# Optimization experiments

Measured on AMD Instinct MI355X. Metric: run time of the kernel, lower is better.

Reference implementation:

```python
import jax, jax.numpy as jnp
import numpy as np

NF = 3
THRESH = 0.05
MODES1 = [0, 64, 32]
MODES2 = [0, 64, 32]
LEVEL = 3
WIDTHS = [32, 64, 64]


def _cgelu(z):
    # split-complex GELU: gelu on real and imag parts independently
    return jax.nn.gelu(z.real) + 1j * jax.nn.gelu(z.imag)


def _forward(x_real, x_imag, Re,
             p_w1_r, p_w1_i, p_b1_r, p_b1_i, p_w2_r, p_w2_i, p_b2_r, p_b2_i,
             w0_r, w0_i, wd1_r, wd1_i, wu1_r, wu1_i, wd2_r, wd2_i, wu2_r, wu2_i,
             S1, S2):
    c = lambda r, i: (r + 1j * i).astype(jnp.complex64)
    x = c(x_real, x_imag)                       # (B, C0, S1, M2) half-spectrum
    B = x.shape[0]
    M1, M2 = S1 // 2, S2 // 2 + 1
    m1_list = [M1, MODES1[1], MODES1[2]]
    m2_list = [M2, MODES2[1], MODES2[2]]

    # --- get_k: fractional powers of signed wavenumbers ---
    h1, h2 = S1 // 2, S2 // 2
    kx1 = jnp.concatenate([jnp.arange(0, S1 - h1), jnp.arange(-h1, 0)]).reshape(S1, 1)
    kx2 = jnp.concatenate([jnp.arange(0, S2 - h2), jnp.arange(-h2, 0)]).reshape(1, S2)
    k = jnp.stack([jnp.broadcast_to(kx1, (S1, S2)),
                   jnp.broadcast_to(kx2, (S1, S2))], 0)[..., :M2]   # (2, S1, M2)
    pw = (jnp.arange(1, NF + 1, dtype=jnp.float32) / NF).reshape(NF, 1, 1, 1)
    k_mat = jnp.power(k[None].astype(jnp.complex64), pw)            # (NF, 2, S1, M2)
    k_mat = jnp.broadcast_to(k_mat.reshape(1, 2 * NF, S1, M2), (B, 2 * NF, S1, M2))

    # --- embed_re: fractional powers of Reynolds number ---
    re_pw = (jnp.arange(1, NF + 1, dtype=jnp.float32) / NF).reshape(1, NF, 1, 1)
    re_mat = jnp.power(Re, re_pw).astype(jnp.complex64)             # (B, NF, 1, 1)
    re_mat = jnp.broadcast_to(re_mat, (B, NF, S1, M2))

    feat = jnp.concatenate([k_mat, re_mat], axis=1)                 # (B, 3*NF, S1, M2)

    # --- complex 1x1-conv MLP p ---
    h = jnp.einsum('bixy,oi->boxy', feat, c(p_w1_r, p_w1_i)) + c(p_b1_r, p_b1_i)[None, :, None, None]
    h = _cgelu(h)
    re_feature = jnp.einsum('bixy,oi->boxy', h, c(p_w2_r, p_w2_i)) + c(p_b2_r, p_b2_i)[None, :, None, None]

    x = x * re_feature
    x = jnp.where(jnp.abs(x) > THRESH, x, jnp.zeros((), x.dtype))   # sparsity mask

    # level 0 (skip_in is all-ones complex)
    x1 = x + 1.0
    x1 = _cgelu(jnp.einsum('bixy,io->boxy', x1, c(w0_r, w0_i)))

    Wd = [None, c(wd1_r, wd1_i), c(wd2_r, wd2_i)]
    Wu = [None, c(wu1_r, wu1_i), c(wu2_r, wu2_i)]

    xs = [x1]
    for i in range(1, LEVEL):  # down path: corner mode truncation + channel mix
        m1, m2 = m1_list[i], m2_list[i]
        x2 = jnp.concatenate([x1[:, :, :m1, :m2], x1[:, :, -m1:, :m2]], axis=2)
        x1 = _cgelu(jnp.einsum('bixy,io->boxy', x2, Wd[i])) + 1.0
        xs.append(x1)

    skip_out = list(xs)
    for i in range(LEVEL - 1, 0, -1):  # up path: channel mix + corner add
        u = _cgelu(jnp.einsum('bixy,io->boxy', xs[i], Wu[i]))
        m1, m2 = m1_list[i], m2_list[i]
        prev = xs[i - 1]
        prev = prev.at[:, :, :m1, :m2].add(u[:, :, :m1, :m2])
        prev = prev.at[:, :, -m1:, :m2].add(u[:, :, -m1:, :m2])
        xs[i - 1] = prev
        skip_out[i - 1] = prev  # torch mutates in place, so skip_out aliases

    return (xs[0], skip_out[0], skip_out[1], skip_out[2])


def setup_inputs() -> dict:
    key = jax.random.key(0)
    B, S1, S2 = 8, 256, 256
    M2 = S2 // 2 + 1
    ks = jax.random.split(key, 24)
    f = lambda k, s: jax.random.normal(k, s, jnp.float32)
    w = lambda k, s: 0.05 * jax.random.normal(k, s, jnp.float32)
    return {
        'x_real': f(ks[0], (B, 32, S1, M2)),
        'x_imag': f(ks[1], (B, 32, S1, M2)),
        'Re': jax.random.uniform(ks[2], (B, 1, 1, 1), jnp.float32, 0.5, 2.0),
        'p_w1_r': w(ks[3], (32, 9)), 'p_w1_i': w(ks[4], (32, 9)),
        'p_b1_r': w(ks[5], (32,)), 'p_b1_i': w(ks[6], (32,)),
        'p_w2_r': w(ks[7], (32, 32)), 'p_w2_i': w(ks[8], (32, 32)),
        'p_b2_r': w(ks[9], (32,)), 'p_b2_i': w(ks[10], (32,)),
        'w0_r': w(ks[11], (32, 32)), 'w0_i': w(ks[12], (32, 32)),
        'wd1_r': w(ks[13], (32, 64)), 'wd1_i': w(ks[14], (32, 64)),
        'wu1_r': w(ks[15], (64, 32)), 'wu1_i': w(ks[16], (64, 32)),
        'wd2_r': w(ks[17], (64, 64)), 'wd2_i': w(ks[18], (64, 64)),
        'wu2_r': w(ks[19], (64, 64)), 'wu2_i': w(ks[20], (64, 64)),
        'S1': S1, 'S2': S2,
    }


def reference(x_real, x_imag, Re,
              p_w1_r, p_w1_i, p_b1_r, p_b1_i, p_w2_r, p_w2_i, p_b2_r, p_b2_i,
              w0_r, w0_i, wd1_r, wd1_i, wu1_r, wu1_i, wd2_r, wd2_i, wu2_r, wu2_i,
              S1, S2):
    return _forward(x_real, x_imag, Re,
                    p_w1_r, p_w1_i, p_b1_r, p_b1_i, p_w2_r, p_w2_i, p_b2_r, p_b2_i,
                    w0_r, w0_i, wd1_r, wd1_i, wu1_r, wu1_i, wd2_r, wd2_i, wu2_r, wu2_i,
                    S1, S2)
```

## Files before the change

### kernel.cpp

```cpp
#include <hip/hip_runtime.h>

typedef long long i64;

#define BB   8
#define SS1  256
#define MM2  129
#define SP0  (SS1*MM2)

#define O0 0LL
#define O1 8454144LL
#define O2 16908288LL
#define O3 21102592LL

__device__ __forceinline__ float ldf(const float* p, i64 i, i64 cap) {
    return (i >= 0 && i < cap) ? p[i] : 0.0f;
}
__device__ __forceinline__ void stf(float* p, i64 i, i64 cap, float v) {
    if (i >= 0 && i < cap) p[i] = v;
}

__device__ __forceinline__ float tanh_fast(float x) {
    float a = fabsf(x);
    float t = __expf(-2.0f * a);
    float r = (1.0f - t) / (1.0f + t);
    return copysignf(r, x);
}
__device__ __forceinline__ float gelu_f(float x) {
    float inner = 0.7978845608028654f * (x + 0.044715f * x * x * x);
    return 0.5f * x * (1.0f + tanh_fast(inner));
}

__device__ __forceinline__ void compute_features(
    int b, int x, int y, const float* __restrict__ Re,
    float* fr, float* fi, float* rp)
{
    float kv0 = (x < 128) ? (float)x : (float)(x - 256);
    float kv1 = (y < 128) ? (float)y : -128.0f;
    const float P[3] = {1.0f/3.0f, 2.0f/3.0f, 1.0f};
    #pragma unroll
    for (int d = 0; d < 2; d++) {
        float k = d ? kv1 : kv0;
        float lg = __logf(fabsf(k));
        #pragma unroll
        for (int f = 0; f < 3; f++) {
            int c = f * 2 + d;
            float m = __expf(P[f] * lg);
            if (k == 0.0f)      { fr[c] = 0.0f; fi[c] = 0.0f; }
            else if (k > 0.0f)  { fr[c] = m;    fi[c] = 0.0f; }
            else {
                float ang = P[f] * 3.14159274101257f;
                fr[c] = m * __cosf(ang);
                fi[c] = m * __sinf(ang);
            }
        }
    }
    float lre = __logf(Re[b]);
    #pragma unroll
    for (int f = 0; f < 3; f++) rp[f] = __expf(P[f] * lre);
}

__device__ __forceinline__ void l0_masked_v(
    int b, int x, int y,
    const float* __restrict__ xr, const float* __restrict__ xi,
    const float* __restrict__ Re,
    const float2* s_w1, const float2* s_b1,
    const float2* s_w2, const float2* s_b2,
    float* vr, float* vi)
{
    float fr[6], fi[6], rp[3];
    compute_features(b, x, y, Re, fr, fi, rp);

    float hr[32], hi[32];
    #pragma unroll
    for (int o = 0; o < 32; o++) {
        float ar = s_b1[o].x, ai = s_b1[o].y;
        #pragma unroll
        for (int i = 0; i < 6; i++) {
            float2 w = s_w1[o * 9 + i];
            ar += w.x * fr[i] - w.y * fi[i];
            ai += w.x * fi[i] + w.y * fr[i];
        }
        #pragma unroll
        for (int i = 0; i < 3; i++) {
            float2 w = s_w1[o * 9 + 6 + i];
            ar += w.x * rp[i];
            ai += w.y * rp[i];
        }
        hr[o] = gelu_f(ar);
        hi[o] = gelu_f(ai);
    }

    i64 base0 = (i64)b * 32 * SP0 + (i64)x * MM2 + y;
    for (int c = 0; c < 32; c++) {
        float rr = s_b2[c].x, ri = s_b2[c].y;
        #pragma unroll
        for (int i = 0; i < 32; i++) {
            float2 w = s_w2[c * 32 + i];
            rr += w.x * hr[i] - w.y * hi[i];
            ri += w.x * hi[i] + w.y * hr[i];
        }
        float xre = xr[base0 + (i64)c * SP0];
        float xim = xi[base0 + (i64)c * SP0];
        float pr = xre * rr - xim * ri;
        float pi = xre * ri + xim * rr;
        if (sqrtf(pr * pr + pi * pi) <= 0.05f) { pr = 0.0f; pi = 0.0f; }
        vr[c] = pr + 1.0f;
        vi[c] = pi;
    }
}

#define STAGE_L0()                                                            \
    for (int t = threadIdx.x; t < 1024; t += 256) {                           \
        s_w2[t] = make_float2(w2r[t], w2i[t]);                                \
        s_w0[t] = make_float2(w0r[t], w0i[t]);                                \
        if (t < 288) s_w1[t] = make_float2(w1r[t], w1i[t]);                   \
        if (t < 32) {                                                         \
            s_b1[t] = make_float2(b1r[t], b1i[t]);                            \
            s_b2[t] = make_float2(b2r[t], b2i[t]);                            \
        }                                                                     \
    }

__global__ __launch_bounds__(256) void k_level0(
    const float* __restrict__ xr, const float* __restrict__ xi,
    const float* __restrict__ Re,
    const float* __restrict__ w1r, const float* __restrict__ w1i,
    const float* __restrict__ b1r, const float* __restrict__ b1i,
    const float* __restrict__ w2r, const float* __restrict__ w2i,
    const float* __restrict__ b2r, const float* __restrict__ b2i,
    const float* __restrict__ w0r, const float* __restrict__ w0i,
    float* __restrict__ of, i64 capf)
{
    __shared__ float2 s_w1[288], s_b1[32], s_w2[1024], s_b2[32], s_w0[1024];
    STAGE_L0();
    __syncthreads();

    int idx = blockIdx.x * 256 + threadIdx.x;
    if (idx >= BB * SP0) return;
    int y  = idx % MM2;
    int t2 = idx / MM2;
    int x  = t2 % SS1;
    int b  = t2 / SS1;

    float vr[32], vi[32];
    l0_masked_v(b, x, y, xr, xi, Re, s_w1, s_b1, s_w2, s_b2, vr, vi);

    i64 base0 = (i64)b * 32 * SP0 + (i64)x * MM2 + y;
    #pragma unroll
    for (int o = 0; o < 32; o++) {
        float a = 0.0f;
        #pragma unroll
        for (int c = 0; c < 32; c++) {
            float2 w = s_w0[c * 32 + o];
            a += w.x * vr[c] - w.y * vi[c];
        }
        float g = gelu_f(a);
        i64 oi = base0 + (i64)o * SP0;
        stf(of, O0 + oi, capf, g);
        stf(of, O1 + oi, capf, g);
    }
}

#define PH  0
#define PV  32
#define PX1 64
#define PV1 96
#define PV2 160

__global__ __launch_bounds__(512, 4) void k_branch1(
    const float* __restrict__ xr, const float* __restrict__ xi,
    const float* __restrict__ Re,
    const float* __restrict__ w1r, const float* __restrict__ w1i,
    const float* __restrict__ b1r, const float* __restrict__ b1i,
    const float* __restrict__ w2r, const float* __restrict__ w2i,
    const float* __restrict__ b2r, const float* __restrict__ b2i,
    const float* __restrict__ w0r, const float* __restrict__ w0i,
    const float* __restrict__ wd1r, const float* __restrict__ wd1i,
    const float* __restrict__ wu1r, const float* __restrict__ wu1i,
    float* __restrict__ of, i64 capf)
{
    int base = blockIdx.x * 8;
    int y0 = base & 63;
    int r1 = (base >> 6) & 127;
    int b  = base >> 13;
    if ((y0 < 32) && (r1 < 32 || r1 >= 96)) return;
    int x0 = (r1 < 64) ? r1 : r1 + 128;

    __shared__ float2 s_w2t[1024];
    __shared__ float2 s_w0[1024];
    __shared__ float2 s_wd1[2048];
    __shared__ float2 s_wu1[2048];
    __shared__ float2 s_pt[8][160];
    __shared__ float  s_u[8][32];

    for (int t = threadIdx.x; t < 1024; t += 512) {
        int c = t >> 5, i = t & 31;
        s_w2t[i * 32 + c] = make_float2(w2r[t], w2i[t]);
        s_w0[t] = make_float2(w0r[t], w0i[t]);
    }
    for (int t = threadIdx.x; t < 2048; t += 512) {
        s_wd1[t] = make_float2(wd1r[t], wd1i[t]);
        s_wu1[t] = make_float2(wu1r[t], wu1i[t]);
    }

    int p = threadIdx.x >> 6;
    int lane = threadIdx.x & 63;
    int y = y0 + p;

    if (lane < 32) {
        float fr[6], fi[6], rp[3];
        compute_features(b, x0, y, Re, fr, fi, rp);
        int o = lane;
        float ar = b1r[o], ai = b1i[o];
        #pragma unroll
        for (int i = 0; i < 6; i++) {
            float wr = w1r[o * 9 + i], wi = w1i[o * 9 + i];
            ar += wr * fr[i] - wi * fi[i];
            ai += wr * fi[i] + wi * fr[i];
        }
        #pragma unroll
        for (int f = 0; f < 3; f++) {
            ar += w1r[o * 9 + 6 + f] * rp[f];
            ai += w1i[o * 9 + 6 + f] * rp[f];
        }
        s_pt[p][PH + o] = make_float2(gelu_f(ar), gelu_f(ai));
    }
    __syncthreads();

    if (lane < 32) {
        int c = lane;
        float rr = b2r[c], ri = b2i[c];
        #pragma unroll
        for (int i = 0; i < 32; i++) {
            float2 w = s_w2t[i * 32 + c];
            float2 h = s_pt[p][PH + i];
            rr += w.x * h.x - w.y * h.y;
            ri += w.x * h.y + w.y * h.x;
        }
        i64 xoff = ((i64)b * 32 + c) * SP0 + (i64)x0 * MM2 + y;
        float xre = xr[xoff], xim = xi[xoff];
        float pr = xre * rr - xim * ri;
        float pi = xre * ri + xim * rr;
        if (sqrtf(pr * pr + pi * pi) <= 0.05f) { pr = 0.0f; pi = 0.0f; }
        s_pt[p][PV + c] = make_float2(pr + 1.0f, pi);
    }
    __syncthreads();

    {
        int o = lane & 31, part = lane >> 5;
        const float* vv = (const float*)&s_pt[p][PV];
        int ia = part ? 1 : 0, ib = part ? 0 : 1;
        float sgn = part ? 1.0f : -1.0f;
        float a = 0.0f;
        #pragma unroll
        for (int c2 = 0; c2 < 32; c2++) {
            float2 w = s_w0[c2 * 32 + o];
            a += w.x * vv[2 * c2 + ia] + sgn * w.y * vv[2 * c2 + ib];
        }
        a = gelu_f(a);
        ((float*)&s_pt[p][PX1 + o])[part] = a;
    }
    __syncthreads();

    {
        float ar = 0.0f, ai = 0.0f;
        #pragma unroll
        for (int i2 = 0; i2 < 32; i2++) {
            float2 w = s_wd1[i2 * 64 + lane];
            float2 x1 = s_pt[p][PX1 + i2];
            ar += w.x * x1.x - w.y * x1.y;
            ai += w.x * x1.y + w.y * x1.x;
        }
        s_pt[p][PV1 + lane] = make_float2(gelu_f(ar) + 1.0f, gelu_f(ai));
    }
    __syncthreads();

    {
        int o = threadIdx.x >> 3, ty = threadIdx.x & 7;
        float v = s_pt[ty][PV1 + o].x;
        stf(of, O2 + ((i64)((i64)b * 64 + o) * 128 + r1) * 64 + (y0 + ty), capf, v);
    }

    {
        int o = lane & 31, half = lane >> 5;
        float acc = 0.0f;
        #pragma unroll
        for (int c2 = 0; c2 < 32; c2++) {
            int c = half * 32 + c2;
            float2 w = s_wu1[c * 32 + o];
            float2 v1 = s_pt[p][PV1 + c];
            acc += w.x * v1.x - w.y * v1.y;
        }
        acc += __shfl_xor(acc, 32);
        if (lane < 32) s_u[p][o] = gelu_f(acc);
    }
    __syncthreads();

    if (threadIdx.x < 256) {
        int o = threadIdx.x >> 3, ty = threadIdx.x & 7;
        i64 oi = ((i64)b * 32 + o) * SP0 + (i64)x0 * MM2 + (y0 + ty);
        float cur = ldf(of, O0 + oi, capf) + s_u[ty][o];
        stf(of, O0 + oi, capf, cur);
        stf(of, O1 + oi, capf, cur);
    }
}

__global__ __launch_bounds__(512, 4) void k_branch2(
    const float* __restrict__ xr, const float* __restrict__ xi,
    const float* __restrict__ Re,
    const float* __restrict__ w1r, const float* __restrict__ w1i,
    const float* __restrict__ b1r, const float* __restrict__ b1i,
    const float* __restrict__ w2r, const float* __restrict__ w2i,
    const float* __restrict__ b2r, const float* __restrict__ b2i,
    const float* __restrict__ w0r, const float* __restrict__ w0i,
    const float* __restrict__ wd1r, const float* __restrict__ wd1i,
    const float* __restrict__ wu1r, const float* __restrict__ wu1i,
    const float* __restrict__ wd2r, const float* __restrict__ wd2i,
    const float* __restrict__ wu2r, const float* __restrict__ wu2i,
    float* __restrict__ of, i64 capf)
{
    int base = blockIdx.x * 8;
    int y0 = base & 31;
    int r2 = (base >> 5) & 63;
    int b  = base >> 11;
    int r1 = (r2 < 32) ? r2 : r2 + 64;
    int x0 = (r1 < 64) ? r1 : r1 + 128;

    __shared__ float2 s_w2t[1024];
    __shared__ float2 s_w0[1024];
    __shared__ float2 s_wd1[2048];
    __shared__ float2 s_wu1[2048];
    __shared__ float2 s_pt[8][224];
    __shared__ float  s_u[8][32];

    for (int t = threadIdx.x; t < 1024; t += 512) {
        int c = t >> 5, i = t & 31;
        s_w2t[i * 32 + c] = make_float2(w2r[t], w2i[t]);
        s_w0[t] = make_float2(w0r[t], w0i[t]);
    }
    for (int t = threadIdx.x; t < 2048; t += 512) {
        s_wd1[t] = make_float2(wd1r[t], wd1i[t]);
        s_wu1[t] = make_float2(wu1r[t], wu1i[t]);
    }

    int p = threadIdx.x >> 6;
    int lane = threadIdx.x & 63;
    int y = y0 + p;

    if (lane < 32) {
        float fr[6], fi[6], rp[3];
        compute_features(b, x0, y, Re, fr, fi, rp);
        int o = lane;
        float ar = b1r[o], ai = b1i[o];
        #pragma unroll
        for (int i = 0; i < 6; i++) {
            float wr = w1r[o * 9 + i], wi = w1i[o * 9 + i];
            ar += wr * fr[i] - wi * fi[i];
            ai += wr * fi[i] + wi * fr[i];
        }
        #pragma unroll
        for (int f = 0; f < 3; f++) {
            ar += w1r[o * 9 + 6 + f] * rp[f];
            ai += w1i[o * 9 + 6 + f] * rp[f];
        }
        s_pt[p][PH + o] = make_float2(gelu_f(ar), gelu_f(ai));
    }
    __syncthreads();

    if (lane < 32) {
        int c = lane;
        float rr = b2r[c], ri = b2i[c];
        #pragma unroll
        for (int i = 0; i < 32; i++) {
            float2 w = s_w2t[i * 32 + c];
            float2 h = s_pt[p][PH + i];
            rr += w.x * h.x - w.y * h.y;
            ri += w.x * h.y + w.y * h.x;
        }
        i64 xoff = ((i64)b * 32 + c) * SP0 + (i64)x0 * MM2 + y;
        float xre = xr[xoff], xim = xi[xoff];
        float pr = xre * rr - xim * ri;
        float pi = xre * ri + xim * rr;
        if (sqrtf(pr * pr + pi * pi) <= 0.05f) { pr = 0.0f; pi = 0.0f; }
        s_pt[p][PV + c] = make_float2(pr + 1.0f, pi);
    }
    __syncthreads();

    {
        int o = lane & 31, part = lane >> 5;
        const float* vv = (const float*)&s_pt[p][PV];
        int ia = part ? 1 : 0, ib = part ? 0 : 1;
        float sgn = part ? 1.0f : -1.0f;
        float a = 0.0f;
        #pragma unroll
        for (int c2 = 0; c2 < 32; c2++) {
            float2 w = s_w0[c2 * 32 + o];
            a += w.x * vv[2 * c2 + ia] + sgn * w.y * vv[2 * c2 + ib];
        }
        a = gelu_f(a);
        ((float*)&s_pt[p][PX1 + o])[part] = a;
    }
    __syncthreads();

    {
        float ar = 0.0f, ai = 0.0f;
        #pragma unroll
        for (int i2 = 0; i2 < 32; i2++) {
            float2 w = s_wd1[i2 * 64 + lane];
            float2 x1 = s_pt[p][PX1 + i2];
            ar += w.x * x1.x - w.y * x1.y;
            ai += w.x * x1.y + w.y * x1.x;
        }
        s_pt[p][PV1 + lane] = make_float2(gelu_f(ar) + 1.0f, gelu_f(ai));
    }
    __syncthreads();

    {
        float ar = 0.0f, ai = 0.0f;
        #pragma unroll 8
        for (int c2 = 0; c2 < 64; c2++) {
            float wr = wd2r[c2 * 64 + lane], wi = wd2i[c2 * 64 + lane];
            float2 v1 = s_pt[p][PV1 + c2];
            ar += wr * v1.x - wi * v1.y;
            ai += wr * v1.y + wi * v1.x;
        }
        s_pt[p][PV2 + lane] = make_float2(gelu_f(ar) + 1.0f, gelu_f(ai));
    }
    __syncthreads();

    {
        int o = threadIdx.x >> 3, ty = threadIdx.x & 7;
        float v = s_pt[ty][PV2 + o].x;
        stf(of, O3 + ((i64)((i64)b * 64 + o) * 64 + r2) * 32 + (y0 + ty), capf, v);
    }

    {
        float ar = 0.0f, ai = 0.0f;
        #pragma unroll 8
        for (int c2 = 0; c2 < 64; c2++) {
            float wr = wu2r[c2 * 64 + lane], wi = wu2i[c2 * 64 + lane];
            float2 v2 = s_pt[p][PV2 + c2];
            ar += wr * v2.x - wi * v2.y;
            ai += wr * v2.y + wi * v2.x;
        }
        float2 v1 = s_pt[p][PV1 + lane];
        v1.x += gelu_f(ar);
        v1.y += gelu_f(ai);
        s_pt[p][PV1 + lane] = v1;
    }
    __syncthreads();

    {
        int o = threadIdx.x >> 3, ty = threadIdx.x & 7;
        float v = s_pt[ty][PV1 + o].x;
        stf(of, O2 + ((i64)((i64)b * 64 + o) * 128 + r1) * 64 + (y0 + ty), capf, v);
    }

    {
        int o = lane & 31, half = lane >> 5;
        float acc = 0.0f;
        #pragma unroll
        for (int c2 = 0; c2 < 32; c2++) {
            int c = half * 32 + c2;
            float2 w = s_wu1[c * 32 + o];
            float2 v1 = s_pt[p][PV1 + c];
            acc += w.x * v1.x - w.y * v1.y;
        }
        acc += __shfl_xor(acc, 32);
        if (lane < 32) s_u[p][o] = gelu_f(acc);
    }
    __syncthreads();

    if (threadIdx.x < 256) {
        int o = threadIdx.x >> 3, ty = threadIdx.x & 7;
        i64 oi = ((i64)b * 32 + o) * SP0 + (i64)x0 * MM2 + (y0 + ty);
        float cur = ldf(of, O0 + oi, capf) + s_u[ty][o];
        stf(of, O0 + oi, capf, cur);
        stf(of, O1 + oi, capf, cur);
    }
}

extern "C" void kernel_launch(void* const* d_in, const int* in_sizes, int n_in,
                              void* d_out, int out_size, void* d_ws, size_t ws_size,
                              hipStream_t stream) {
    const float* xr   = (const float*)d_in[0];
    const float* xi   = (const float*)d_in[1];
    const float* Re   = (const float*)d_in[2];
    const float* w1r  = (const float*)d_in[3];
    const float* w1i  = (const float*)d_in[4];
    const float* b1r  = (const float*)d_in[5];
    const float* b1i  = (const float*)d_in[6];
    const float* w2r  = (const float*)d_in[7];
    const float* w2i  = (const float*)d_in[8];
    const float* b2r  = (const float*)d_in[9];
    const float* b2i  = (const float*)d_in[10];
    const float* w0r  = (const float*)d_in[11];
    const float* w0i  = (const float*)d_in[12];
    const float* wd1r = (const float*)d_in[13];
    const float* wd1i = (const float*)d_in[14];
    const float* wu1r = (const float*)d_in[15];
    const float* wu1i = (const float*)d_in[16];
    const float* wd2r = (const float*)d_in[17];
    const float* wd2i = (const float*)d_in[18];
    const float* wu2r = (const float*)d_in[19];
    const float* wu2i = (const float*)d_in[20];

    float* of  = (float*)d_out;
    i64 capf   = (i64)out_size;

    k_level0<<<dim3((BB * SP0 + 255) / 256), 256, 0, stream>>>(
        xr, xi, Re, w1r, w1i, b1r, b1i, w2r, w2i, b2r, b2i, w0r, w0i, of, capf);
    k_branch1<<<dim3(8192), 512, 0, stream>>>(
        xr, xi, Re, w1r, w1i, b1r, b1i, w2r, w2i, b2r, b2i, w0r, w0i,
        wd1r, wd1i, wu1r, wu1i, of, capf);
    k_branch2<<<dim3(2048), 512, 0, stream>>>(
        xr, xi, Re, w1r, w1i, b1r, b1i, w2r, w2i, b2r, b2i, w0r, w0i,
        wd1r, wd1i, wu1r, wu1i, wd2r, wd2i, wu2r, wu2i, of, capf);
}
```

Before: 566.9 us.

## Restructure level-0 kernel to stream channels and read weights directly from global

The level-0 kernel drops LDS weight staging and the block-wide barrier, reading weights directly through global/scalar loads since they are uniform across the wave. It fuses the masked-value computation with the w0 projection by accumulating 32 outputs per input channel, so the 64-entry vr/vi arrays no longer need to be held. Reduction chains are split into two partial sums. Elsewhere, sqrt in the mask test becomes a squared-threshold comparison, and tanh uses a hardware reciprocal instead of division, which changes rounding slightly.

```diff
diff --git a/kernel.cpp b/kernel.cpp
--- a/kernel.cpp
+++ b/kernel.cpp
@@ -22,7 +22,7 @@
 __device__ __forceinline__ float tanh_fast(float x) {
     float a = fabsf(x);
     float t = __expf(-2.0f * a);
-    float r = (1.0f - t) / (1.0f + t);
+    float r = (1.0f - t) * __builtin_amdgcn_rcpf(1.0f + t);
     return copysignf(r, x);
 }
 __device__ __forceinline__ float gelu_f(float x) {
@@ -59,67 +59,6 @@
     for (int f = 0; f < 3; f++) rp[f] = __expf(P[f] * lre);
 }
 
-__device__ __forceinline__ void l0_masked_v(
-    int b, int x, int y,
-    const float* __restrict__ xr, const float* __restrict__ xi,
-    const float* __restrict__ Re,
-    const float2* s_w1, const float2* s_b1,
-    const float2* s_w2, const float2* s_b2,
-    float* vr, float* vi)
-{
-    float fr[6], fi[6], rp[3];
-    compute_features(b, x, y, Re, fr, fi, rp);
-
-    float hr[32], hi[32];
-    #pragma unroll
-    for (int o = 0; o < 32; o++) {
-        float ar = s_b1[o].x, ai = s_b1[o].y;
-        #pragma unroll
-        for (int i = 0; i < 6; i++) {
-            float2 w = s_w1[o * 9 + i];
-            ar += w.x * fr[i] - w.y * fi[i];
-            ai += w.x * fi[i] + w.y * fr[i];
-        }
-        #pragma unroll
-        for (int i = 0; i < 3; i++) {
-            float2 w = s_w1[o * 9 + 6 + i];
-            ar += w.x * rp[i];
-            ai += w.y * rp[i];
-        }
-        hr[o] = gelu_f(ar);
-        hi[o] = gelu_f(ai);
-    }
-
-    i64 base0 = (i64)b * 32 * SP0 + (i64)x * MM2 + y;
-    for (int c = 0; c < 32; c++) {
-        float rr = s_b2[c].x, ri = s_b2[c].y;
-        #pragma unroll
-        for (int i = 0; i < 32; i++) {
-            float2 w = s_w2[c * 32 + i];
-            rr += w.x * hr[i] - w.y * hi[i];
-            ri += w.x * hi[i] + w.y * hr[i];
-        }
-        float xre = xr[base0 + (i64)c * SP0];
-        float xim = xi[base0 + (i64)c * SP0];
-        float pr = xre * rr - xim * ri;
-        float pi = xre * ri + xim * rr;
-        if (sqrtf(pr * pr + pi * pi) <= 0.05f) { pr = 0.0f; pi = 0.0f; }
-        vr[c] = pr + 1.0f;
-        vi[c] = pi;
-    }
-}
-
-#define STAGE_L0()                                                            \
-    for (int t = threadIdx.x; t < 1024; t += 256) {                           \
-        s_w2[t] = make_float2(w2r[t], w2i[t]);                                \
-        s_w0[t] = make_float2(w0r[t], w0i[t]);                                \
-        if (t < 288) s_w1[t] = make_float2(w1r[t], w1i[t]);                   \
-        if (t < 32) {                                                         \
-            s_b1[t] = make_float2(b1r[t], b1i[t]);                            \
-            s_b2[t] = make_float2(b2r[t], b2i[t]);                            \
-        }                                                                     \
-    }
-
 __global__ __launch_bounds__(256) void k_level0(
     const float* __restrict__ xr, const float* __restrict__ xi,
     const float* __restrict__ Re,
@@ -130,10 +69,6 @@
     const float* __restrict__ w0r, const float* __restrict__ w0i,
     float* __restrict__ of, i64 capf)
 {
-    __shared__ float2 s_w1[288], s_b1[32], s_w2[1024], s_b2[32], s_w0[1024];
-    STAGE_L0();
-    __syncthreads();
-
     int idx = blockIdx.x * 256 + threadIdx.x;
     if (idx >= BB * SP0) return;
     int y  = idx % MM2;
@@ -141,19 +76,66 @@
     int x  = t2 % SS1;
     int b  = t2 / SS1;
 
-    float vr[32], vi[32];
-    l0_masked_v(b, x, y, xr, xi, Re, s_w1, s_b1, s_w2, s_b2, vr, vi);
-
-    i64 base0 = (i64)b * 32 * SP0 + (i64)x * MM2 + y;
+    float fr[6], fi[6], rp[3];
+    compute_features(b, x, y, Re, fr, fi, rp);
+
+    float hr[32], hi[32];
     #pragma unroll
     for (int o = 0; o < 32; o++) {
-        float a = 0.0f;
-        #pragma unroll
-        for (int c = 0; c < 32; c++) {
-            float2 w = s_w0[c * 32 + o];
-            a += w.x * vr[c] - w.y * vi[c];
-        }
-        float g = gelu_f(a);
+        float ar = b1r[o], ai = b1i[o];
+        #pragma unroll
+        for (int i = 0; i < 6; i++) {
+            float wr = w1r[o * 9 + i], wi = w1i[o * 9 + i];
+            ar += wr * fr[i] - wi * fi[i];
+            ai += wr * fi[i] + wi * fr[i];
+        }
+        #pragma unroll
+        for (int f = 0; f < 3; f++) {
+            ar += w1r[o * 9 + 6 + f] * rp[f];
+            ai += w1i[o * 9 + 6 + f] * rp[f];
+        }
+        hr[o] = gelu_f(ar);
+        hi[o] = gelu_f(ai);
+    }
+
+    float acc[32];
+    #pragma unroll
+    for (int o = 0; o < 32; o++) acc[o] = 0.0f;
+
+    const float TH2 = 0.05f * 0.05f;
+    i64 base0 = (i64)b * 32 * SP0 + (i64)x * MM2 + y;
+    for (int c = 0; c < 32; c++) {
+        float rr0 = b2r[c], ri0 = b2i[c], rr1 = 0.0f, ri1 = 0.0f;
+        #pragma unroll
+        for (int i = 0; i < 16; i++) {
+            float wr = w2r[c * 32 + i], wi = w2i[c * 32 + i];
+            rr0 += wr * hr[i] - wi * hi[i];
+            ri0 += wr * hi[i] + wi * hr[i];
+        }
+        #pragma unroll
+        for (int i = 16; i < 32; i++) {
+            float wr = w2r[c * 32 + i], wi = w2i[c * 32 + i];
+            rr1 += wr * hr[i] - wi * hi[i];
+            ri1 += wr * hi[i] + wi * hr[i];
+        }
+        float rrs = rr0 + rr1, ris = ri0 + ri1;
+        float xre = xr[base0 + (i64)c * SP0];
+        float xim = xi[base0 + (i64)c * SP0];
+        float pr = xre * rrs - xim * ris;
+        float pi = xre * ris + xim * rrs;
+        if (pr * pr + pi * pi <= TH2) { pr = 0.0f; pi = 0.0f; }
+        float vr_c = pr + 1.0f;
+        float vi_c = pi;
+        #pragma unroll
+        for (int o = 0; o < 32; o++) {
+            float wr = w0r[c * 32 + o], wi = w0i[c * 32 + o];
+            acc[o] += wr * vr_c - wi * vi_c;
+        }
+    }
+
+    #pragma unroll
+    for (int o = 0; o < 32; o++) {
+        float g = gelu_f(acc[o]);
         i64 oi = base0 + (i64)o * SP0;
         stf(of, O0 + oi, capf, g);
         stf(of, O1 + oi, capf, g);
@@ -240,7 +222,8 @@
         float xre = xr[xoff], xim = xi[xoff];
         float pr = xre * rr - xim * ri;
         float pi = xre * ri + xim * rr;
-        if (sqrtf(pr * pr + pi * pi) <= 0.05f) { pr = 0.0f; pi = 0.0f; }
+        const float TH2 = 0.05f * 0.05f;
+        if (pr * pr + pi * pi <= TH2) { pr = 0.0f; pi = 0.0f; }
         s_pt[p][PV + c] = make_float2(pr + 1.0f, pi);
     }
     __syncthreads();
@@ -380,7 +363,8 @@
         float xre = xr[xoff], xim = xi[xoff];
         float pr = xre * rr - xim * ri;
         float pi = xre * ri + xim * rr;
-        if (sqrtf(pr * pr + pi * pi) <= 0.05f) { pr = 0.0f; pi = 0.0f; }
+        const float TH2 = 0.05f * 0.05f;
+        if (pr * pr + pi * pi <= TH2) { pr = 0.0f; pi = 0.0f; }
         s_pt[p][PV + c] = make_float2(pr + 1.0f, pi);
     }
     __syncthreads();
```

Result: faster. 529.9 us (-6.5%).
